# Kernel tuning notes

Measured on AMD Instinct MI355X. Metric: run time of the kernel, lower is better.

## Reference

```python
import jax, jax.numpy as jnp
import numpy as np

TEMP = 0.07
EPS = 1e-12  # F.normalize eps

def _l2norm(x, axis):
    n = jnp.sqrt(jnp.sum(x * x, axis=axis, keepdims=True))
    return x / jnp.maximum(n, EPS)

def setup_inputs() -> dict:
    key = jax.random.key(0)
    features = jax.random.normal(key, (128, 2048), dtype=jnp.float32)
    return {"features": features}

def reference(features):
    # features: [B, D] raw backbone features (pre-normalization)
    f = _l2norm(features, axis=1)                      # [B, D]
    B = f.shape[0]
    fi = f[:, None, :]                                  # [B, 1, D] -> broadcasts over j
    fj = f[None, :, :]                                  # [1, B, D] -> broadcasts over i
    mutual = fi * fj                                    # 'ik,jk->ijk'  [B, B, D]
    gate_i = fi * mutual                                # 'ik,ijk->ijk'
    gate_j = fj * mutual                                # 'jk,ijk->ijk'
    # NOTE: '+ features_raw' on an [B,B,D] tensor broadcasts features_raw as [1,B,D], i.e. adds f[j]
    feat_self_i  = _l2norm(fi * gate_i + fj, axis=2)    # [B, B, D]
    feat_other_i = _l2norm(fi * gate_j + fj, axis=2)
    feat_other_j = _l2norm(fj * gate_i + fj, axis=2)
    # (feat_self_j = normalize(fj*gate_j + fj) is computed in the source but never used in the loss)
    d_self_i  = jnp.einsum('ik,ijk->ij', f, feat_self_i)  / TEMP   # [B, B]
    d_self_j  = jnp.einsum('ik,ijk->ij', f, feat_other_j) / TEMP   # source dots against features_other_j
    d_other_i = jnp.einsum('ik,ijk->ij', f, feat_other_i) / TEMP
    d_other_j = d_self_j                                            # identical einsum in source
    e_si, e_sj, e_oi, e_oj = (jnp.exp(d) for d in (d_self_i, d_self_j, d_other_i, d_other_j))
    vs_all = jnp.sum(e_si + e_sj + e_oi + e_oj, axis=1, keepdims=True)  # [B, 1]
    log_prob = d_self_i - jnp.log(vs_all)               # [B, B]
    mean_log_prob_pos = jnp.sum(log_prob, axis=1) / B
    loss = -jnp.mean(mean_log_prob_pos)
    return loss
```

## Files before the change

### kernel.cpp

```cpp
#include <hip/hip_runtime.h>
#include <math.h>

#define B_ 128
#define K_ 2048
#define TEMP_ 0.07f
#define EPS_ 1e-12f
#define NBLK_ 1024

__global__ __launch_bounds__(256, 4) void k_pairs(const float* __restrict__ feat,
                                                  float* __restrict__ part) {
    const int blk = blockIdx.x;
    const int i = blk >> 3;
    const int jg = blk & 7;
    const int tid = threadIdx.x;
    const int wave = tid >> 6, lane = tid & 63;
    const int s = lane & 15;
    const int grp = lane >> 4;

    __shared__ float sa[K_];
    __shared__ float sg[K_];
    __shared__ float wsum[4];

    {
        const float4* fi4 = reinterpret_cast<const float4*>(feat + (size_t)i * K_);
        float4 v0 = fi4[tid];
        float4 v1 = fi4[tid + 256];
        float ss = v0.x * v0.x + v0.y * v0.y + v0.z * v0.z + v0.w * v0.w
                 + v1.x * v1.x + v1.y * v1.y + v1.z * v1.z + v1.w * v1.w;
#pragma unroll
        for (int o = 1; o < 64; o <<= 1) ss += __shfl_xor(ss, o, 64);
        if (lane == 0) wsum[wave] = ss;
        __syncthreads();
        const float tot = wsum[0] + wsum[1] + wsum[2] + wsum[3];
        const float rn = 1.0f / fmaxf(sqrtf(tot), EPS_);

        float4* a4w = reinterpret_cast<float4*>(sa);
        float4* g4w = reinterpret_cast<float4*>(sg);
#define STAGE(V, IDX)                                                   \
        {                                                               \
            float4 a, g;                                                \
            a.x = (V).x * rn; a.y = (V).y * rn;                         \
            a.z = (V).z * rn; a.w = (V).w * rn;                         \
            g.x = 1.0f + a.x * a.x * a.x; g.y = 1.0f + a.y * a.y * a.y; \
            g.z = 1.0f + a.z * a.z * a.z; g.w = 1.0f + a.w * a.w * a.w; \
            a4w[IDX] = a; g4w[IDX] = g;                                 \
        }
        STAGE(v0, tid)
        STAGE(v1, tid + 256)
#undef STAGE
    }
    __syncthreads();

    const int j = jg * 16 + wave * 4 + grp;
    const float4* bj = reinterpret_cast<const float4*>(feat + (size_t)j * K_);
    const float4* a4 = reinterpret_cast<const float4*>(sa);
    const float4* g4 = reinterpret_cast<const float4*>(sg);

    float du = 0.f, uu = 0.f, sab = 0.f, saq = 0.f, sqq = 0.f, sqb = 0.f, sbb = 0.f;

#pragma unroll 8
    for (int c = 0; c < 32; ++c) {
        const int idx = c * 16 + s;
        const float4 a = a4[idx];
        const float4 g = g4[idx];
        const float4 b = bj[idx];
#define ACC1(AX, GX, BX)                             \
        {                                            \
            const float w = (BX) * (GX);             \
            du  = fmaf((AX), w, du);                 \
            uu  = fmaf(w, w, uu);                    \
            const float p = (AX) * (BX);             \
            sab += p;                                \
            const float q = p * p;                   \
            saq = fmaf((AX), q, saq);                \
            sqq = fmaf(q, q, sqq);                   \
            sqb = fmaf(q, (BX), sqb);                \
            sbb = fmaf((BX), (BX), sbb);             \
        }
        ACC1(a.x, g.x, b.x)
        ACC1(a.y, g.y, b.y)
        ACC1(a.z, g.z, b.z)
        ACC1(a.w, g.w, b.w)
#undef ACC1
    }

#pragma unroll
    for (int o = 1; o < 16; o <<= 1) {
        du  += __shfl_xor(du,  o, 64);
        uu  += __shfl_xor(uu,  o, 64);
        sab += __shfl_xor(sab, o, 64);
        saq += __shfl_xor(saq, o, 64);
        sqq += __shfl_xor(sqq, o, 64);
        sqb += __shfl_xor(sqb, o, 64);
        sbb += __shfl_xor(sbb, o, 64);
    }

    const float inv_t = 1.0f / TEMP_;
    const float ds = du / fmaxf(sqrtf(uu), EPS_) * inv_t;
    const float c  = 1.0f / fmaxf(sqrtf(sbb), EPS_);
    const float dv = fmaf(c, saq, sab);
    const float vv = fmaf(c * c, sqq, fmaf(2.0f * c, sqb, sbb));
    const float dn = dv / fmaxf(sqrtf(vv), EPS_) * inv_t;
    float s1 = ds;
    float s2 = __expf(ds) + 3.0f * __expf(dn);

    s1 += __shfl_xor(s1, 16, 64); s1 += __shfl_xor(s1, 32, 64);
    s2 += __shfl_xor(s2, 16, 64); s2 += __shfl_xor(s2, 32, 64);

    __shared__ float p1[4], p2[4];
    if (lane == 0) { p1[wave] = s1; p2[wave] = s2; }
    __syncthreads();
    if (tid == 0) {
        part[blk * 2 + 0] = p1[0] + p1[1] + p1[2] + p1[3];
        part[blk * 2 + 1] = p2[0] + p2[1] + p2[2] + p2[3];
    }
}

__global__ __launch_bounds__(128) void k_final(const float* __restrict__ part,
                                               float* __restrict__ out) {
    const int i = threadIdx.x;
    float s1 = 0.0f, s2 = 0.0f;
#pragma unroll
    for (int q = 0; q < 8; ++q) {
        s1 += part[(i * 8 + q) * 2 + 0];
        s2 += part[(i * 8 + q) * 2 + 1];
    }
    float c = s1 * (1.0f / B_) - __logf(s2);
#pragma unroll
    for (int o = 1; o < 64; o <<= 1) c += __shfl_xor(c, o, 64);
    __shared__ float wsum[2];
    const int wave = i >> 6, lane = i & 63;
    if (lane == 0) wsum[wave] = c;
    __syncthreads();
    if (i == 0) out[0] = -(wsum[0] + wsum[1]) * (1.0f / B_);
}

extern "C" void kernel_launch(void* const* d_in, const int* in_sizes, int n_in,
                              void* d_out, int out_size, void* d_ws, size_t ws_size,
                              hipStream_t stream) {
    const float* feat = (const float*)d_in[0];
    float* part = (float*)d_ws;
    float* out = (float*)d_out;

    k_pairs<<<NBLK_, 256, 0, stream>>>(feat, part);
    k_final<<<1, 128, 0, stream>>>(part, out);
}
```

Before: 21.32 us.

## Process two i-rows per block to reuse each j-row load

Each block now stages two normalized i-rows (and their gates) in shared memory and handles 8 j-rows, with 32 lanes per j instead of 16. Each global load of a j-row feeds accumulators for both i-rows, and the j-row norm is computed once for both. This halves global j-row traffic per pair. In exchange, shared memory doubles to 32 KB per block, register pressure rises with 13 accumulators, and the final kernel reduces 16 partials per row instead of 8.

After: 24.04 us. 12.8% more time.

```diff
diff --git a/kernel.cpp b/kernel.cpp
--- a/kernel.cpp
+++ b/kernel.cpp
@@ -10,32 +10,38 @@
 __global__ __launch_bounds__(256, 4) void k_pairs(const float* __restrict__ feat,
                                                   float* __restrict__ part) {
     const int blk = blockIdx.x;
-    const int i = blk >> 3;
-    const int jg = blk & 7;
+    const int ip = blk >> 4;
+    const int jg = blk & 15;
+    const int i0 = ip * 2;
     const int tid = threadIdx.x;
     const int wave = tid >> 6, lane = tid & 63;
-    const int s = lane & 15;
-    const int grp = lane >> 4;
+    const int l32 = lane & 31;
 
-    __shared__ float sa[K_];
-    __shared__ float sg[K_];
+    __shared__ float sa0[K_], sg0[K_], sa1[K_], sg1[K_];
     __shared__ float wsum[4];
+    __shared__ float sp[4][4];
 
     {
-        const float4* fi4 = reinterpret_cast<const float4*>(feat + (size_t)i * K_);
-        float4 v0 = fi4[tid];
-        float4 v1 = fi4[tid + 256];
-        float ss = v0.x * v0.x + v0.y * v0.y + v0.z * v0.z + v0.w * v0.w
-                 + v1.x * v1.x + v1.y * v1.y + v1.z * v1.z + v1.w * v1.w;
+        const int half = tid >> 7;
+        const int t = tid & 127;
+        const float4* row4 = reinterpret_cast<const float4*>(feat + (size_t)(i0 + half) * K_);
+        float4 v0 = row4[t];
+        float4 v1 = row4[t + 128];
+        float4 v2 = row4[t + 256];
+        float4 v3 = row4[t + 384];
+        float ss = v0.x*v0.x + v0.y*v0.y + v0.z*v0.z + v0.w*v0.w
+                 + v1.x*v1.x + v1.y*v1.y + v1.z*v1.z + v1.w*v1.w
+                 + v2.x*v2.x + v2.y*v2.y + v2.z*v2.z + v2.w*v2.w
+                 + v3.x*v3.x + v3.y*v3.y + v3.z*v3.z + v3.w*v3.w;
 #pragma unroll
         for (int o = 1; o < 64; o <<= 1) ss += __shfl_xor(ss, o, 64);
         if (lane == 0) wsum[wave] = ss;
         __syncthreads();
-        const float tot = wsum[0] + wsum[1] + wsum[2] + wsum[3];
+        const float tot = wsum[half * 2] + wsum[half * 2 + 1];
         const float rn = 1.0f / fmaxf(sqrtf(tot), EPS_);
 
-        float4* a4w = reinterpret_cast<float4*>(sa);
-        float4* g4w = reinterpret_cast<float4*>(sg);
+        float4* a4w = reinterpret_cast<float4*>(half ? sa1 : sa0);
+        float4* g4w = reinterpret_cast<float4*>(half ? sg1 : sg0);
 #define STAGE(V, IDX)                                                   \
         {                                                               \
             float4 a, g;                                                \
@@ -45,74 +51,114 @@
             g.z = 1.0f + a.z * a.z * a.z; g.w = 1.0f + a.w * a.w * a.w; \
             a4w[IDX] = a; g4w[IDX] = g;                                 \
         }
-        STAGE(v0, tid)
-        STAGE(v1, tid + 256)
+        STAGE(v0, t)
+        STAGE(v1, t + 128)
+        STAGE(v2, t + 256)
+        STAGE(v3, t + 384)
 #undef STAGE
     }
     __syncthreads();
 
-    const int j = jg * 16 + wave * 4 + grp;
+    const int j = jg * 8 + wave * 2 + (lane >> 5);
     const float4* bj = reinterpret_cast<const float4*>(feat + (size_t)j * K_);
-    const float4* a4 = reinterpret_cast<const float4*>(sa);
-    const float4* g4 = reinterpret_cast<const float4*>(sg);
+    const float4* a04 = reinterpret_cast<const float4*>(sa0);
+    const float4* g04 = reinterpret_cast<const float4*>(sg0);
+    const float4* a14 = reinterpret_cast<const float4*>(sa1);
+    const float4* g14 = reinterpret_cast<const float4*>(sg1);
 
-    float du = 0.f, uu = 0.f, sab = 0.f, saq = 0.f, sqq = 0.f, sqb = 0.f, sbb = 0.f;
+    float du0 = 0.f, uu0 = 0.f, sab0 = 0.f, saq0 = 0.f, sqq0 = 0.f, sqb0 = 0.f;
+    float du1 = 0.f, uu1 = 0.f, sab1 = 0.f, saq1 = 0.f, sqq1 = 0.f, sqb1 = 0.f;
+    float sbb = 0.f;
 
-#pragma unroll 8
-    for (int c = 0; c < 32; ++c) {
-        const int idx = c * 16 + s;
-        const float4 a = a4[idx];
-        const float4 g = g4[idx];
-        const float4 b = bj[idx];
-#define ACC1(AX, GX, BX)                             \
-        {                                            \
-            const float w = (BX) * (GX);             \
-            du  = fmaf((AX), w, du);                 \
-            uu  = fmaf(w, w, uu);                    \
-            const float p = (AX) * (BX);             \
-            sab += p;                                \
-            const float q = p * p;                   \
-            saq = fmaf((AX), q, saq);                \
-            sqq = fmaf(q, q, sqq);                   \
-            sqb = fmaf(q, (BX), sqb);                \
-            sbb = fmaf((BX), (BX), sbb);             \
+#pragma unroll 4
+    for (int it = 0; it < 16; ++it) {
+        const int idx = it * 32 + l32;
+        const float4 b  = bj[idx];
+        const float4 a0 = a04[idx];
+        const float4 g0 = g04[idx];
+        const float4 a1 = a14[idx];
+        const float4 g1 = g14[idx];
+#define ACC1(AX, GX, BX, DU, UU, SAB, SAQ, SQQ, SQB)   \
+        {                                              \
+            const float w = (BX) * (GX);               \
+            DU  = fmaf((AX), w, DU);                   \
+            UU  = fmaf(w, w, UU);                      \
+            const float p = (AX) * (BX);               \
+            SAB += p;                                  \
+            const float q = p * p;                     \
+            SAQ = fmaf((AX), q, SAQ);                  \
+            SQQ = fmaf(q, q, SQQ);                     \
+            SQB = fmaf(q, (BX), SQB);                  \
         }
-        ACC1(a.x, g.x, b.x)
-        ACC1(a.y, g.y, b.y)
-        ACC1(a.z, g.z, b.z)
-        ACC1(a.w, g.w, b.w)
+#define ACCE(C)                                                              \
+        ACC1(a0.C, g0.C, b.C, du0, uu0, sab0, saq0, sqq0, sqb0)              \
+        ACC1(a1.C, g1.C, b.C, du1, uu1, sab1, saq1, sqq1, sqb1)              \
+        sbb = fmaf(b.C, b.C, sbb);
+        ACCE(x)
+        ACCE(y)
+        ACCE(z)
+        ACCE(w)
+#undef ACCE
 #undef ACC1
     }
 
 #pragma unroll
-    for (int o = 1; o < 16; o <<= 1) {
-        du  += __shfl_xor(du,  o, 64);
-        uu  += __shfl_xor(uu,  o, 64);
-        sab += __shfl_xor(sab, o, 64);
-        saq += __shfl_xor(saq, o, 64);
-        sqq += __shfl_xor(sqq, o, 64);
-        sqb += __shfl_xor(sqb, o, 64);
-        sbb += __shfl_xor(sbb, o, 64);
+    for (int o = 1; o < 32; o <<= 1) {
+        du0  += __shfl_xor(du0,  o, 64);
+        uu0  += __shfl_xor(uu0,  o, 64);
+        sab0 += __shfl_xor(sab0, o, 64);
+        saq0 += __shfl_xor(saq0, o, 64);
+        sqq0 += __shfl_xor(sqq0, o, 64);
+        sqb0 += __shfl_xor(sqb0, o, 64);
+        du1  += __shfl_xor(du1,  o, 64);
+        uu1  += __shfl_xor(uu1,  o, 64);
+        sab1 += __shfl_xor(sab1, o, 64);
+        saq1 += __shfl_xor(saq1, o, 64);
+        sqq1 += __shfl_xor(sqq1, o, 64);
+        sqb1 += __shfl_xor(sqb1, o, 64);
+        sbb  += __shfl_xor(sbb,  o, 64);
     }
 
     const float inv_t = 1.0f / TEMP_;
-    const float ds = du / fmaxf(sqrtf(uu), EPS_) * inv_t;
     const float c  = 1.0f / fmaxf(sqrtf(sbb), EPS_);
-    const float dv = fmaf(c, saq, sab);
-    const float vv = fmaf(c * c, sqq, fmaf(2.0f * c, sqb, sbb));
-    const float dn = dv / fmaxf(sqrtf(vv), EPS_) * inv_t;
-    float s1 = ds;
-    float s2 = __expf(ds) + 3.0f * __expf(dn);
+    const float c2 = c * c, tc = 2.0f * c;
 
-    s1 += __shfl_xor(s1, 16, 64); s1 += __shfl_xor(s1, 32, 64);
-    s2 += __shfl_xor(s2, 16, 64); s2 += __shfl_xor(s2, 32, 64);
+    const float ds0 = du0 / fmaxf(sqrtf(uu0), EPS_) * inv_t;
+    const float dv0 = fmaf(c, saq0, sab0);
+    const float vv0 = fmaf(c2, sqq0, fmaf(tc, sqb0, sbb));
+    const float dn0 = dv0 / fmaxf(sqrtf(vv0), EPS_) * inv_t;
+    float s1_0 = ds0;
+    float s2_0 = __expf(ds0) + 3.0f * __expf(dn0);
 
-    __shared__ float p1[4], p2[4];
-    if (lane == 0) { p1[wave] = s1; p2[wave] = s2; }
+    const float ds1 = du1 / fmaxf(sqrtf(uu1), EPS_) * inv_t;
+    const float dv1 = fmaf(c, saq1, sab1);
+    const float vv1 = fmaf(c2, sqq1, fmaf(tc, sqb1, sbb));
+    const float dn1 = dv1 / fmaxf(sqrtf(vv1), EPS_) * inv_t;
+    float s1_1 = ds1;
+    float s2_1 = __expf(ds1) + 3.0f * __expf(dn1);
+
+    s1_0 += __shfl_xor(s1_0, 32, 64);
+    s2_0 += __shfl_xor(s2_0, 32, 64);
+    s1_1 += __shfl_xor(s1_1, 32, 64);
+    s2_1 += __shfl_xor(s2_1, 32, 64);
+
+    if (lane == 0) {
+        sp[wave][0] = s1_0; sp[wave][1] = s2_0;
+        sp[wave][2] = s1_1; sp[wave][3] = s2_1;
+    }
     __syncthreads();
     if (tid == 0) {
-        part[blk * 2 + 0] = p1[0] + p1[1] + p1[2] + p1[3];
-        part[blk * 2 + 1] = p2[0] + p2[1] + p2[2] + p2[3];
+        const int i1 = i0 + 1;
+        float a0 = 0.f, b0 = 0.f, a1 = 0.f, b1 = 0.f;
+#pragma unroll
+        for (int w = 0; w < 4; ++w) {
+            a0 += sp[w][0]; b0 += sp[w][1];
+            a1 += sp[w][2]; b1 += sp[w][3];
+        }
+        part[(i0 * 16 + jg) * 2 + 0] = a0;
+        part[(i0 * 16 + jg) * 2 + 1] = b0;
+        part[(i1 * 16 + jg) * 2 + 0] = a1;
+        part[(i1 * 16 + jg) * 2 + 1] = b1;
     }
 }
 
@@ -121,9 +167,9 @@
     const int i = threadIdx.x;
     float s1 = 0.0f, s2 = 0.0f;
 #pragma unroll
-    for (int q = 0; q < 8; ++q) {
-        s1 += part[(i * 8 + q) * 2 + 0];
-        s2 += part[(i * 8 + q) * 2 + 1];
+    for (int q = 0; q < 16; ++q) {
+        s1 += part[(i * 16 + q) * 2 + 0];
+        s2 += part[(i * 16 + q) * 2 + 1];
     }
     float c = s1 * (1.0f / B_) - __logf(s2);
 #pragma unroll
```
